# Optimization experiments

Hardware: AMD Instinct MI355X
Metric: run time of the kernel (lower is better)

Reference implementation:

```python
import math
import jax, jax.numpy as jnp
import numpy as np


def _procrustes_R(H):
    # H: [B, 3, 3]. Rotation R = V @ U^T with reflection fix (det(R) >= 0),
    # matching torch.svd convention (v = V, not V^T).
    u, s, vh = jnp.linalg.svd(H)
    v = jnp.swapaxes(vh, -1, -2)                       # [B,3,3]
    r = jnp.einsum('bij,bkj->bik', v, u)               # V @ U^T
    det = jnp.linalg.det(r)                            # [B]
    sign = jnp.where(det < 0, -1.0, 1.0)               # flip last column of V (reflect = diag(1,1,-1))
    flip = jnp.stack([jnp.ones_like(sign), jnp.ones_like(sign), sign], axis=-1)[:, None, :]
    v = v * flip
    return jnp.einsum('bij,bkj->bik', v, u)


def setup_inputs() -> dict:
    key = jax.random.key(0)
    k1, k2, k3, k4 = jax.random.split(key, 4)
    B, D, N, M = 8, 512, 2048, 2048
    return {
        'src_embedding': jax.random.normal(k1, (B, D, N), dtype=jnp.float32),
        'tgt_embedding': jax.random.normal(k2, (B, D, M), dtype=jnp.float32),
        'src': jax.random.normal(k3, (B, 3, N), dtype=jnp.float32),
        'tgt': jax.random.normal(k4, (B, 3, M), dtype=jnp.float32),
    }


def reference(src_embedding, tgt_embedding, src, tgt):
    d_k = src_embedding.shape[1]
    # attention correspondence: scores[b,n,m]
    scores = jnp.einsum('bdn,bdm->bnm', src_embedding, tgt_embedding) / math.sqrt(d_k)
    scores = jax.nn.softmax(scores, axis=2)
    # soft correspondence of src points in tgt: [B,3,N]
    src_corr = jnp.einsum('bdm,bnm->bdn', tgt, scores)
    src_mean = src.mean(axis=2, keepdims=True)          # [B,3,1]
    src_centered = src - src_mean
    src_corr_centered = src_corr - src_corr.mean(axis=2, keepdims=True)
    H = jnp.einsum('bin,bjn->bij', src_centered, src_corr_centered)  # [B,3,3]
    R = _procrustes_R(H)
    t = jnp.einsum('bij,bjk->bik', -R, src_mean) + tgt.mean(axis=2, keepdims=True)
    return R, t.reshape(src.shape[0], 3)
```

## Files before the change

### kernel.cpp

```cpp
#include <hip/hip_runtime.h>
#include <hip/hip_bf16.h>

#define BQ 8
#define DIM 512
#define NN 2048
#define MM 2048
#define MSPLIT 16

typedef __attribute__((ext_vector_type(8))) short short8;
typedef __attribute__((ext_vector_type(8))) unsigned short ushort8;
typedef __attribute__((ext_vector_type(4))) float floatx4;

#define GLOAD_LDS(gp, lp) \
    __builtin_amdgcn_global_load_lds( \
        (const __attribute__((address_space(1))) void*)(gp), \
        (__attribute__((address_space(3))) void*)(lp), 16, 0, 0)


static __device__ __forceinline__ unsigned short f2bf(float x) {
    __hip_bfloat16 h = __float2bfloat16(x);
    return *(unsigned short*)&h;
}

__global__ __launch_bounds__(256) void transpose_cast_kernel(
    const float* __restrict__ src_emb,
    const float* __restrict__ tgt_emb,
    __hip_bfloat16* __restrict__ Abf,
    __hip_bfloat16* __restrict__ Bbf)
{
    const int n0 = blockIdx.x * 64;
    const int d0 = blockIdx.y * 64;
    const int b  = blockIdx.z & 7;
    const int which = blockIdx.z >> 3;

    const float* in = (which == 0 ? src_emb : tgt_emb) + (size_t)b * DIM * NN;
    __hip_bfloat16* out = (which == 0 ? Abf : Bbf) + (size_t)b * NN * DIM;

    __shared__ float tl[64][65];

    const int t = threadIdx.x;

    {
        const int u = t & 15;
        const int r = t >> 4;
        #pragma unroll
        for (int rr = r; rr < 64; rr += 16) {
            float4 v = *(const float4*)&in[(size_t)(d0 + rr) * NN + n0 + u * 4];
            tl[rr][u * 4 + 0] = v.x;
            tl[rr][u * 4 + 1] = v.y;
            tl[rr][u * 4 + 2] = v.z;
            tl[rr][u * 4 + 3] = v.w;
        }
    }
    __syncthreads();

    {
        const int u = t & 7;
        const int r = t >> 3;
        #pragma unroll
        for (int rn = r; rn < 64; rn += 32) {
            ushort8 o;
            #pragma unroll
            for (int j = 0; j < 8; j++)
                o[j] = f2bf(tl[u * 8 + j][rn]);
            *(ushort8*)&out[(size_t)(n0 + rn) * DIM + d0 + u * 8] = o;
        }
    }
}

__global__ __launch_bounds__(512, 2) void attn_mfma_kernel(
    const __hip_bfloat16* __restrict__ Abf,
    const __hip_bfloat16* __restrict__ Bbf,
    const float* __restrict__ tgt,
    float* __restrict__ part)
{
    const int nt = blockIdx.x;
    const int qt = blockIdx.y;
    const int b  = blockIdx.z;
    const int t  = threadIdx.x;
    const int wave = t >> 6;
    const int lane = t & 63;
    const int lm   = lane & 15;
    const int quad = lane >> 4;
    const int wn   = wave * 32;
    const int bw   = wave * 16;

    __shared__ short As[256 * 64];
    __shared__ short Bs[128 * 64];

    const __hip_bfloat16* Abase = Abf + ((size_t)(b * NN + nt * 256)) * DIM;
    const int m0 = qt * 128;
    const __hip_bfloat16* Bbase = Bbf + ((size_t)(b * MM + m0)) * DIM;
    const float* Tb = tgt + (size_t)b * 3 * MM;

    const float SCALE = 0.044194173824159216f * 1.4426950408889634f;

    const int r8 = lane >> 3;
    const int c8 = lane & 7;
    const int cc = c8 ^ r8;
    const __hip_bfloat16* gA = Abase + (size_t)(wn + r8) * DIM + cc * 8;
    const __hip_bfloat16* gB = Bbase + (size_t)(bw + r8) * DIM + cc * 8;
    short* lA = &As[wn * 64];
    short* lB = &Bs[bw * 64];

    floatx4 acc[2][8];
    #pragma unroll
    for (int i = 0; i < 2; i++)
        #pragma unroll
        for (int j = 0; j < 8; j++)
            acc[i][j] = (floatx4){0.f, 0.f, 0.f, 0.f};

    #pragma unroll
    for (int kt = 0; kt < 8; kt++) {
        #pragma unroll
        for (int i = 0; i < 4; i++)
            GLOAD_LDS(gA + kt * 64 + (size_t)i * 8 * DIM, lA + i * 512);
        #pragma unroll
        for (int i = 0; i < 2; i++)
            GLOAD_LDS(gB + kt * 64 + (size_t)i * 8 * DIM, lB + i * 512);
        __syncthreads();

        #pragma unroll
        for (int ks = 0; ks < 2; ks++) {
            const int pc = (((ks * 4 + quad) ^ (lane & 7)) * 8);
            short8 af0 = *(const short8*)&As[(wn +      lm) * 64 + pc];
            short8 af1 = *(const short8*)&As[(wn + 16 + lm) * 64 + pc];
            #pragma unroll
            for (int j = 0; j < 8; j++) {
                short8 bf = *(const short8*)&Bs[(j * 16 + lm) * 64 + pc];
                acc[0][j] = __builtin_amdgcn_mfma_f32_16x16x32_bf16(af0, bf, acc[0][j], 0, 0, 0);
                acc[1][j] = __builtin_amdgcn_mfma_f32_16x16x32_bf16(af1, bf, acc[1][j], 0, 0, 0);
            }
        }
        __syncthreads();
    }

    float v0[8], v1[8], v2[8];
    #pragma unroll
    for (int j = 0; j < 8; j++) {
        int vc = m0 + j * 16 + lm;
        v0[j] = Tb[vc];
        v1[j] = Tb[MM + vc];
        v2[j] = Tb[2 * MM + vc];
    }

    const size_t slot = (size_t)(b * MSPLIT + qt) * NN;
    #pragma unroll
    for (int i = 0; i < 2; i++) {
        float l4[4] = {0,0,0,0};
        float o0[4] = {0,0,0,0};
        float o1[4] = {0,0,0,0};
        float o2[4] = {0,0,0,0};
        #pragma unroll
        for (int j = 0; j < 8; j++) {
            #pragma unroll
            for (int r = 0; r < 4; r++) {
                float e = __builtin_amdgcn_exp2f(acc[i][j][r] * SCALE);
                l4[r] += e;
                o0[r] += e * v0[j];
                o1[r] += e * v1[j];
                o2[r] += e * v2[j];
            }
        }
        #pragma unroll
        for (int m = 1; m <= 8; m <<= 1) {
            #pragma unroll
            for (int r = 0; r < 4; r++) {
                l4[r] += __shfl_xor(l4[r], m);
                o0[r] += __shfl_xor(o0[r], m);
                o1[r] += __shfl_xor(o1[r], m);
                o2[r] += __shfl_xor(o2[r], m);
            }
        }
        if (lm == 0) {
            #pragma unroll
            for (int r = 0; r < 4; r++) {
                int n = nt * 256 + wn + i * 16 + quad * 4 + r;
                ((float4*)part)[slot + n] = make_float4(l4[r], o0[r], o1[r], o2[r]);
            }
        }
    }
}

__global__ __launch_bounds__(128) void reduce1_kernel(
    const float* __restrict__ part,
    const float* __restrict__ src,
    const float* __restrict__ tgt,
    float* __restrict__ red)
{
    const int chunk = blockIdx.x;
    const int b     = blockIdx.y;
    const int t     = threadIdx.x;
    const int n     = chunk * 128 + t;

    const float4* w4 = (const float4*)part;
    const float* S = src + (size_t)b * 3 * NN;
    const float* T = tgt + (size_t)b * 3 * MM;

    float l = 0.f, y0 = 0.f, y1 = 0.f, y2 = 0.f;
    #pragma unroll
    for (int q = 0; q < 16; q++) {
        float4 p = w4[(size_t)(b * 16 + q) * NN + n];
        l += p.x; y0 += p.y; y1 += p.z; y2 += p.w;
    }
    float inv = 1.0f / l;
    float c0 = y0 * inv, c1 = y1 * inv, c2 = y2 * inv;
    float s0 = S[n], s1 = S[NN + n], s2 = S[2 * NN + n];

    float vals[18];
    vals[0] = s0;  vals[1] = s1;  vals[2] = s2;
    vals[3] = c0;  vals[4] = c1;  vals[5] = c2;
    vals[6] = T[n]; vals[7] = T[MM + n]; vals[8] = T[2 * MM + n];
    vals[9]  = s0 * c0; vals[10] = s0 * c1; vals[11] = s0 * c2;
    vals[12] = s1 * c0; vals[13] = s1 * c1; vals[14] = s1 * c2;
    vals[15] = s2 * c0; vals[16] = s2 * c1; vals[17] = s2 * c2;

    #pragma unroll
    for (int m = 1; m <= 32; m <<= 1)
        #pragma unroll
        for (int c = 0; c < 18; c++)
            vals[c] += __shfl_xor(vals[c], m);

    __shared__ float w0[18];
    if (t == 64)
        #pragma unroll
        for (int c = 0; c < 18; c++) w0[c] = vals[c];
    __syncthreads();
    if (t == 0)
        #pragma unroll
        for (int c = 0; c < 18; c++)
            red[(size_t)(b * 16 + chunk) * 18 + c] = vals[c] + w0[c];
}

__global__ __launch_bounds__(64) void procrustes_kernel(
    const float* __restrict__ red,
    float* __restrict__ out)
{
    const int b = blockIdx.x;
    const int t = threadIdx.x;

    __shared__ float res[18];
    if (t < 18) {
        float a = 0.f;
        #pragma unroll
        for (int q = 0; q < 16; q++)
            a += red[(size_t)(b * 16 + q) * 18 + t];
        res[t] = a;
    }
    __syncthreads();

    if (t == 0) {
        const float invN = 1.0f / (float)NN;
        float mus[3], muc[3], mut[3], H[3][3];
        for (int i = 0; i < 3; i++) {
            mus[i] = res[i] * invN;
            muc[i] = res[3 + i] * invN;
            mut[i] = res[6 + i] * invN;
        }
        for (int i = 0; i < 3; i++)
            for (int j = 0; j < 3; j++)
                H[i][j] = res[9 + i * 3 + j] - (float)NN * mus[i] * muc[j];

        float A[3][3];
        for (int i = 0; i < 3; i++)
            for (int j = 0; j < 3; j++)
                A[i][j] = H[0][i] * H[0][j] + H[1][i] * H[1][j] + H[2][i] * H[2][j];

        float V[3][3] = {{1,0,0},{0,1,0},{0,0,1}};
        for (int sweep = 0; sweep < 6; sweep++) {
            for (int pi = 0; pi < 3; pi++) {
                int p = (pi < 2) ? 0 : 1;
                int q = (pi == 0) ? 1 : 2;
                float apq = A[p][q];
                if (fabsf(apq) < 1e-30f) continue;
                float tau = (A[q][q] - A[p][p]) / (2.0f * apq);
                float tt = (tau >= 0.0f) ? 1.0f / (tau + sqrtf(1.0f + tau * tau))
                                         : -1.0f / (-tau + sqrtf(1.0f + tau * tau));
                float c = 1.0f / sqrtf(1.0f + tt * tt);
                float s = tt * c;
                for (int k = 0; k < 3; k++) {
                    float akp = A[k][p], akq = A[k][q];
                    A[k][p] = c * akp - s * akq;
                    A[k][q] = s * akp + c * akq;
                }
                for (int k = 0; k < 3; k++) {
                    float apk = A[p][k], aqk = A[q][k];
                    A[p][k] = c * apk - s * aqk;
                    A[q][k] = s * apk + c * aqk;
                }
                for (int k = 0; k < 3; k++) {
                    float vkp = V[k][p], vkq = V[k][q];
                    V[k][p] = c * vkp - s * vkq;
                    V[k][q] = s * vkp + c * vkq;
                }
            }
        }

        float lam[3] = {A[0][0], A[1][1], A[2][2]};
        int idx[3] = {0, 1, 2};
        for (int a = 0; a < 2; a++)
            for (int bb = 0; bb < 2 - a; bb++)
                if (lam[idx[bb]] < lam[idx[bb + 1]]) { int tmp = idx[bb]; idx[bb] = idx[bb + 1]; idx[bb + 1] = tmp; }

        float Vc[3][3], U[3][3];
        for (int c = 0; c < 3; c++) {
            float sv = sqrtf(fmaxf(lam[idx[c]], 0.0f));
            float isv = 1.0f / fmaxf(sv, 1e-20f);
            for (int r = 0; r < 3; r++) {
                Vc[r][c] = V[r][idx[c]];
                U[r][c] = (H[r][0] * V[0][idx[c]] + H[r][1] * V[1][idx[c]] + H[r][2] * V[2][idx[c]]) * isv;
            }
        }

        {
            float nrm = rsqrtf(U[0][0]*U[0][0] + U[1][0]*U[1][0] + U[2][0]*U[2][0]);
            for (int r = 0; r < 3; r++) U[r][0] *= nrm;
            float d01 = U[0][0]*U[0][1] + U[1][0]*U[1][1] + U[2][0]*U[2][1];
            for (int r = 0; r < 3; r++) U[r][1] -= d01 * U[r][0];
            nrm = rsqrtf(U[0][1]*U[0][1] + U[1][1]*U[1][1] + U[2][1]*U[2][1]);
            for (int r = 0; r < 3; r++) U[r][1] *= nrm;
            float d02 = U[0][0]*U[0][2] + U[1][0]*U[1][2] + U[2][0]*U[2][2];
            float d12 = U[0][1]*U[0][2] + U[1][1]*U[1][2] + U[2][1]*U[2][2];
            for (int r = 0; r < 3; r++) U[r][2] -= d02 * U[r][0] + d12 * U[r][1];
            nrm = rsqrtf(U[0][2]*U[0][2] + U[1][2]*U[1][2] + U[2][2]*U[2][2]);
            for (int r = 0; r < 3; r++) U[r][2] *= nrm;
        }

        float det = H[0][0]*(H[1][1]*H[2][2] - H[1][2]*H[2][1])
                  - H[0][1]*(H[1][0]*H[2][2] - H[1][2]*H[2][0])
                  + H[0][2]*(H[1][0]*H[2][1] - H[1][1]*H[2][0]);
        float sgn = (det < 0.0f) ? -1.0f : 1.0f;

        float R[3][3];
        for (int i = 0; i < 3; i++)
            for (int j = 0; j < 3; j++)
                R[i][j] = Vc[i][0]*U[j][0] + Vc[i][1]*U[j][1] + sgn * Vc[i][2]*U[j][2];

        for (int i = 0; i < 3; i++)
            for (int j = 0; j < 3; j++)
                out[b * 9 + i * 3 + j] = R[i][j];
        for (int i = 0; i < 3; i++)
            out[BQ * 9 + b * 3 + i] = mut[i] - (R[i][0]*mus[0] + R[i][1]*mus[1] + R[i][2]*mus[2]);
    }
}

extern "C" void kernel_launch(void* const* d_in, const int* in_sizes, int n_in,
                              void* d_out, int out_size, void* d_ws, size_t ws_size,
                              hipStream_t stream) {
    const float* src_emb = (const float*)d_in[0];
    const float* tgt_emb = (const float*)d_in[1];
    const float* src     = (const float*)d_in[2];
    const float* tgt     = (const float*)d_in[3];
    float* out = (float*)d_out;

    float* part = (float*)d_ws;
    __hip_bfloat16* Abf = (__hip_bfloat16*)((char*)d_ws + (4 << 20));
    __hip_bfloat16* Bbf = (__hip_bfloat16*)((char*)d_ws + (20 << 20));
    float* red = (float*)((char*)d_ws + (36 << 20));

    dim3 gridT(NN / 64, DIM / 64, 2 * BQ);
    transpose_cast_kernel<<<gridT, 256, 0, stream>>>(src_emb, tgt_emb, Abf, Bbf);

    dim3 gridA(NN / 256, MSPLIT, BQ);
    attn_mfma_kernel<<<gridA, 512, 0, stream>>>(Abf, Bbf, tgt, part);

    dim3 gridR(16, BQ);
    reduce1_kernel<<<gridR, 128, 0, stream>>>(part, src, tgt, red);

    procrustes_kernel<<<BQ, 64, 0, stream>>>(red, out);
}
```

Measured before the change: 166.7 us.

## Double-buffer LDS tiles and enlarge attention tile to 256x256 per block

The attention MFMA kernel now processes a 256x256 score tile per block with a 4x2 wave layout (64x128 per wave) instead of 256x128. It double-buffers A and B in LDS, prefetching the next K slice while computing the current one, using explicit vmcnt waits and raw barriers, and raises wave priority around the MFMA loop. This aims to hide global load latency and improve operand reuse per LDS read. The cost is 128KB of LDS per block and 128 accumulator registers per lane, which likely cuts occupancy below the declared two blocks per CU.

```diff
diff --git a/kernel.cpp b/kernel.cpp
--- a/kernel.cpp
+++ b/kernel.cpp
@@ -5,7 +5,6 @@
 #define DIM 512
 #define NN 2048
 #define MM 2048
-#define MSPLIT 16
 
 typedef __attribute__((ext_vector_type(8))) short short8;
 typedef __attribute__((ext_vector_type(8))) unsigned short ushort8;
@@ -82,14 +81,15 @@
     const int lane = t & 63;
     const int lm   = lane & 15;
     const int quad = lane >> 4;
-    const int wn   = wave * 32;
-    const int bw   = wave * 16;
-
-    __shared__ short As[256 * 64];
-    __shared__ short Bs[128 * 64];
+    const int wn = (wave >> 1) * 64;
+    const int wm = (wave & 1) * 128;
+    const int sr = wave * 32;
+
+    __shared__ short As[2][256 * 64];
+    __shared__ short Bs[2][256 * 64];
 
     const __hip_bfloat16* Abase = Abf + ((size_t)(b * NN + nt * 256)) * DIM;
-    const int m0 = qt * 128;
+    const int m0 = qt * 256;
     const __hip_bfloat16* Bbase = Bbf + ((size_t)(b * MM + m0)) * DIM;
     const float* Tb = tgt + (size_t)b * 3 * MM;
 
@@ -98,55 +98,78 @@
     const int r8 = lane >> 3;
     const int c8 = lane & 7;
     const int cc = c8 ^ r8;
-    const __hip_bfloat16* gA = Abase + (size_t)(wn + r8) * DIM + cc * 8;
-    const __hip_bfloat16* gB = Bbase + (size_t)(bw + r8) * DIM + cc * 8;
-    short* lA = &As[wn * 64];
-    short* lB = &Bs[bw * 64];
-
-    floatx4 acc[2][8];
-    #pragma unroll
-    for (int i = 0; i < 2; i++)
+    const __hip_bfloat16* gA = Abase + (size_t)(sr + r8) * DIM + cc * 8;
+    const __hip_bfloat16* gB = Bbase + (size_t)(sr + r8) * DIM + cc * 8;
+
+#define STAGE(p, kt) do { \
+        short* lAp = &As[p][sr * 64]; \
+        short* lBp = &Bs[p][sr * 64]; \
+        _Pragma("unroll") \
+        for (int i_ = 0; i_ < 4; i_++) { \
+            GLOAD_LDS(gA + (kt) * 64 + (size_t)i_ * 8 * DIM, lAp + i_ * 512); \
+            GLOAD_LDS(gB + (kt) * 64 + (size_t)i_ * 8 * DIM, lBp + i_ * 512); \
+        } \
+    } while (0)
+
+    floatx4 acc[4][8];
+    #pragma unroll
+    for (int i = 0; i < 4; i++)
         #pragma unroll
         for (int j = 0; j < 8; j++)
             acc[i][j] = (floatx4){0.f, 0.f, 0.f, 0.f};
 
+    STAGE(0, 0);
+
     #pragma unroll
     for (int kt = 0; kt < 8; kt++) {
-        #pragma unroll
-        for (int i = 0; i < 4; i++)
-            GLOAD_LDS(gA + kt * 64 + (size_t)i * 8 * DIM, lA + i * 512);
-        #pragma unroll
-        for (int i = 0; i < 2; i++)
-            GLOAD_LDS(gB + kt * 64 + (size_t)i * 8 * DIM, lB + i * 512);
-        __syncthreads();
-
+        const int cur = kt & 1;
+        if (kt < 7) {
+            STAGE(cur ^ 1, kt + 1);
+            asm volatile("s_waitcnt vmcnt(8)" ::: "memory");
+        } else {
+            asm volatile("s_waitcnt vmcnt(0)" ::: "memory");
+        }
+        __builtin_amdgcn_s_barrier();
+
+        const short* Ac = &As[cur][0];
+        const short* Bc = &Bs[cur][0];
+        __builtin_amdgcn_s_setprio(1);
         #pragma unroll
         for (int ks = 0; ks < 2; ks++) {
             const int pc = (((ks * 4 + quad) ^ (lane & 7)) * 8);
-            short8 af0 = *(const short8*)&As[(wn +      lm) * 64 + pc];
-            short8 af1 = *(const short8*)&As[(wn + 16 + lm) * 64 + pc];
+            short8 af[4];
+            #pragma unroll
+            for (int i = 0; i < 4; i++)
+                af[i] = *(const short8*)&Ac[(wn + i * 16 + lm) * 64 + pc];
             #pragma unroll
             for (int j = 0; j < 8; j++) {
-                short8 bf = *(const short8*)&Bs[(j * 16 + lm) * 64 + pc];
-                acc[0][j] = __builtin_amdgcn_mfma_f32_16x16x32_bf16(af0, bf, acc[0][j], 0, 0, 0);
-                acc[1][j] = __builtin_amdgcn_mfma_f32_16x16x32_bf16(af1, bf, acc[1][j], 0, 0, 0);
-            }
-        }
-        __syncthreads();
-    }
+                short8 bf = *(const short8*)&Bc[(wm + j * 16 + lm) * 64 + pc];
+                #pragma unroll
+                for (int i = 0; i < 4; i++)
+                    acc[i][j] = __builtin_amdgcn_mfma_f32_16x16x32_bf16(af[i], bf, acc[i][j], 0, 0, 0);
+            }
+        }
+        __builtin_amdgcn_s_setprio(0);
+
+        if (kt < 7) {
+            asm volatile("s_waitcnt lgkmcnt(0)" ::: "memory");
+            __builtin_amdgcn_s_barrier();
+        }
+    }
+#undef STAGE
 
     float v0[8], v1[8], v2[8];
     #pragma unroll
     for (int j = 0; j < 8; j++) {
-        int vc = m0 + j * 16 + lm;
+        int vc = m0 + wm + j * 16 + lm;
         v0[j] = Tb[vc];
         v1[j] = Tb[MM + vc];
         v2[j] = Tb[2 * MM + vc];
     }
 
-    const size_t slot = (size_t)(b * MSPLIT + qt) * NN;
-    #pragma unroll
-    for (int i = 0; i < 2; i++) {
+    const size_t slot = (size_t)(b * 16 + qt * 2 + (wave & 1)) * NN;
+    #pragma unroll
+    for (int i = 0; i < 4; i++) {
         float l4[4] = {0,0,0,0};
         float o0[4] = {0,0,0,0};
         float o1[4] = {0,0,0,0};
@@ -361,7 +384,7 @@
     dim3 gridT(NN / 64, DIM / 64, 2 * BQ);
     transpose_cast_kernel<<<gridT, 256, 0, stream>>>(src_emb, tgt_emb, Abf, Bbf);
 
-    dim3 gridA(NN / 256, MSPLIT, BQ);
+    dim3 gridA(NN / 256, MM / 256, BQ);
     attn_mfma_kernel<<<gridA, 512, 0, stream>>>(Abf, Bbf, tgt, part);
 
     dim3 gridR(16, BQ);
```

Result: no change. 167.3 us (+0.4%).

## Retile attention GEMM to 128x128 with K=128 stages and merge reduction kernels

Applied to the files above, without the earlier changes.

The attention kernel moves from 256x128 tiles with 512 threads and K-steps of 64 to 128x128 tiles with 256 threads and K-steps of 128. This halves the number of barrier-synchronised K iterations and doubles the grid size. The separate reduce and Procrustes kernels are merged into one 256-thread-per-batch finish kernel, which saves a launch and an intermediate buffer. The trade-offs are less A reuse per block, since B traffic per output doubles relative to A, a larger LDS footprint of 64KB that may limit occupancy, and a serial finish with only 8 blocks.

```diff
diff --git a/kernel.cpp b/kernel.cpp
--- a/kernel.cpp
+++ b/kernel.cpp
@@ -5,7 +5,6 @@
 #define DIM 512
 #define NN 2048
 #define MM 2048
-#define MSPLIT 16
 
 typedef __attribute__((ext_vector_type(8))) short short8;
 typedef __attribute__((ext_vector_type(8))) unsigned short ushort8;
@@ -68,7 +67,7 @@
     }
 }
 
-__global__ __launch_bounds__(512, 2) void attn_mfma_kernel(
+__global__ __launch_bounds__(256, 2) void attn_mfma_kernel(
     const __hip_bfloat16* __restrict__ Abf,
     const __hip_bfloat16* __restrict__ Bbf,
     const float* __restrict__ tgt,
@@ -83,25 +82,20 @@
     const int lm   = lane & 15;
     const int quad = lane >> 4;
     const int wn   = wave * 32;
-    const int bw   = wave * 16;
-
-    __shared__ short As[256 * 64];
-    __shared__ short Bs[128 * 64];
-
-    const __hip_bfloat16* Abase = Abf + ((size_t)(b * NN + nt * 256)) * DIM;
+
+    __shared__ short As[128 * 128];
+    __shared__ short Bs[128 * 128];
+
+    const __hip_bfloat16* Abase = Abf + ((size_t)(b * NN + nt * 128)) * DIM;
     const int m0 = qt * 128;
     const __hip_bfloat16* Bbase = Bbf + ((size_t)(b * MM + m0)) * DIM;
     const float* Tb = tgt + (size_t)b * 3 * MM;
 
     const float SCALE = 0.044194173824159216f * 1.4426950408889634f;
 
-    const int r8 = lane >> 3;
+    const int lr = lane >> 4;
+    const int hh = (lane >> 3) & 1;
     const int c8 = lane & 7;
-    const int cc = c8 ^ r8;
-    const __hip_bfloat16* gA = Abase + (size_t)(wn + r8) * DIM + cc * 8;
-    const __hip_bfloat16* gB = Bbase + (size_t)(bw + r8) * DIM + cc * 8;
-    short* lA = &As[wn * 64];
-    short* lB = &Bs[bw * 64];
 
     floatx4 acc[2][8];
     #pragma unroll
@@ -111,23 +105,26 @@
             acc[i][j] = (floatx4){0.f, 0.f, 0.f, 0.f};
 
     #pragma unroll
-    for (int kt = 0; kt < 8; kt++) {
-        #pragma unroll
-        for (int i = 0; i < 4; i++)
-            GLOAD_LDS(gA + kt * 64 + (size_t)i * 8 * DIM, lA + i * 512);
-        #pragma unroll
-        for (int i = 0; i < 2; i++)
-            GLOAD_LDS(gB + kt * 64 + (size_t)i * 8 * DIM, lB + i * 512);
+    for (int kt = 0; kt < 4; kt++) {
+        #pragma unroll
+        for (int it = 0; it < 8; it++) {
+            const int row = wave * 32 + it * 4 + lr;
+            const size_t goff = (size_t)row * DIM + kt * 128 + hh * 64
+                              + (c8 ^ (row & 7)) * 8;
+            GLOAD_LDS(Abase + goff, &As[(wave * 32 + it * 4) * 128]);
+            GLOAD_LDS(Bbase + goff, &Bs[(wave * 32 + it * 4) * 128]);
+        }
         __syncthreads();
 
         #pragma unroll
-        for (int ks = 0; ks < 2; ks++) {
-            const int pc = (((ks * 4 + quad) ^ (lane & 7)) * 8);
-            short8 af0 = *(const short8*)&As[(wn +      lm) * 64 + pc];
-            short8 af1 = *(const short8*)&As[(wn + 16 + lm) * 64 + pc];
+        for (int ks = 0; ks < 4; ks++) {
+            const int col = (ks >> 1) * 64
+                          + ((((ks & 1) * 4 + quad) ^ (lm & 7)) * 8);
+            short8 af0 = *(const short8*)&As[(wn + lm) * 128 + col];
+            short8 af1 = *(const short8*)&As[(wn + 16 + lm) * 128 + col];
             #pragma unroll
             for (int j = 0; j < 8; j++) {
-                short8 bf = *(const short8*)&Bs[(j * 16 + lm) * 64 + pc];
+                short8 bf = *(const short8*)&Bs[(j * 16 + lm) * 128 + col];
                 acc[0][j] = __builtin_amdgcn_mfma_f32_16x16x32_bf16(af0, bf, acc[0][j], 0, 0, 0);
                 acc[1][j] = __builtin_amdgcn_mfma_f32_16x16x32_bf16(af1, bf, acc[1][j], 0, 0, 0);
             }
@@ -144,7 +141,7 @@
         v2[j] = Tb[2 * MM + vc];
     }
 
-    const size_t slot = (size_t)(b * MSPLIT + qt) * NN;
+    const size_t slot = (size_t)(b * 16 + qt) * NN;
     #pragma unroll
     for (int i = 0; i < 2; i++) {
         float l4[4] = {0,0,0,0};
@@ -175,81 +172,70 @@
         if (lm == 0) {
             #pragma unroll
             for (int r = 0; r < 4; r++) {
-                int n = nt * 256 + wn + i * 16 + quad * 4 + r;
+                int n = nt * 128 + wn + i * 16 + quad * 4 + r;
                 ((float4*)part)[slot + n] = make_float4(l4[r], o0[r], o1[r], o2[r]);
             }
         }
     }
 }
 
-__global__ __launch_bounds__(128) void reduce1_kernel(
+__global__ __launch_bounds__(256) void finish_kernel(
     const float* __restrict__ part,
     const float* __restrict__ src,
     const float* __restrict__ tgt,
-    float* __restrict__ red)
-{
-    const int chunk = blockIdx.x;
-    const int b     = blockIdx.y;
-    const int t     = threadIdx.x;
-    const int n     = chunk * 128 + t;
-
-    const float4* w4 = (const float4*)part;
-    const float* S = src + (size_t)b * 3 * NN;
-    const float* T = tgt + (size_t)b * 3 * MM;
-
-    float l = 0.f, y0 = 0.f, y1 = 0.f, y2 = 0.f;
-    #pragma unroll
-    for (int q = 0; q < 16; q++) {
-        float4 p = w4[(size_t)(b * 16 + q) * NN + n];
-        l += p.x; y0 += p.y; y1 += p.z; y2 += p.w;
-    }
-    float inv = 1.0f / l;
-    float c0 = y0 * inv, c1 = y1 * inv, c2 = y2 * inv;
-    float s0 = S[n], s1 = S[NN + n], s2 = S[2 * NN + n];
-
-    float vals[18];
-    vals[0] = s0;  vals[1] = s1;  vals[2] = s2;
-    vals[3] = c0;  vals[4] = c1;  vals[5] = c2;
-    vals[6] = T[n]; vals[7] = T[MM + n]; vals[8] = T[2 * MM + n];
-    vals[9]  = s0 * c0; vals[10] = s0 * c1; vals[11] = s0 * c2;
-    vals[12] = s1 * c0; vals[13] = s1 * c1; vals[14] = s1 * c2;
-    vals[15] = s2 * c0; vals[16] = s2 * c1; vals[17] = s2 * c2;
-
-    #pragma unroll
-    for (int m = 1; m <= 32; m <<= 1)
-        #pragma unroll
-        for (int c = 0; c < 18; c++)
-            vals[c] += __shfl_xor(vals[c], m);
-
-    __shared__ float w0[18];
-    if (t == 64)
-        #pragma unroll
-        for (int c = 0; c < 18; c++) w0[c] = vals[c];
-    __syncthreads();
-    if (t == 0)
-        #pragma unroll
-        for (int c = 0; c < 18; c++)
-            red[(size_t)(b * 16 + chunk) * 18 + c] = vals[c] + w0[c];
-}
-
-__global__ __launch_bounds__(64) void procrustes_kernel(
-    const float* __restrict__ red,
     float* __restrict__ out)
 {
     const int b = blockIdx.x;
     const int t = threadIdx.x;
-
-    __shared__ float res[18];
-    if (t < 18) {
-        float a = 0.f;
-        #pragma unroll
-        for (int q = 0; q < 16; q++)
-            a += red[(size_t)(b * 16 + q) * 18 + t];
-        res[t] = a;
-    }
+    const int wave = t >> 6;
+    const int lane = t & 63;
+
+    const float4* w4 = (const float4*)part;
+    const float* S = src + (size_t)b * 3 * NN;
+    const float* T = tgt + (size_t)b * 3 * MM;
+
+    float vals[18];
+    #pragma unroll
+    for (int c = 0; c < 18; c++) vals[c] = 0.f;
+
+    for (int k = 0; k < 8; k++) {
+        const int n = t + k * 256;
+        float l = 0.f, y0 = 0.f, y1 = 0.f, y2 = 0.f;
+        #pragma unroll
+        for (int q = 0; q < 16; q++) {
+            float4 p = w4[(size_t)(b * 16 + q) * NN + n];
+            l += p.x; y0 += p.y; y1 += p.z; y2 += p.w;
+        }
+        float inv = 1.0f / l;
+        float c0 = y0 * inv, c1 = y1 * inv, c2 = y2 * inv;
+        float s0 = S[n], s1 = S[NN + n], s2 = S[2 * NN + n];
+
+        vals[0] += s0;  vals[1] += s1;  vals[2] += s2;
+        vals[3] += c0;  vals[4] += c1;  vals[5] += c2;
+        vals[6] += T[n]; vals[7] += T[MM + n]; vals[8] += T[2 * MM + n];
+        vals[9]  += s0 * c0; vals[10] += s0 * c1; vals[11] += s0 * c2;
+        vals[12] += s1 * c0; vals[13] += s1 * c1; vals[14] += s1 * c2;
+        vals[15] += s2 * c0; vals[16] += s2 * c1; vals[17] += s2 * c2;
+    }
+
+    #pragma unroll
+    for (int m = 1; m <= 32; m <<= 1)
+        #pragma unroll
+        for (int c = 0; c < 18; c++)
+            vals[c] += __shfl_xor(vals[c], m);
+
+    __shared__ float wsum[4][18];
+    if (lane == 0)
+        #pragma unroll
+        for (int c = 0; c < 18; c++) wsum[wave][c] = vals[c];
     __syncthreads();
 
     if (t == 0) {
+        float res[18];
+        #pragma unroll
+        for (int c = 0; c < 18; c++)
+            res[c] = wsum[0][c] + wsum[1][c] + wsum[2][c] + wsum[3][c];
+
         const float invN = 1.0f / (float)NN;
         float mus[3], muc[3], mut[3], H[3][3];
         for (int i = 0; i < 3; i++) {
@@ -356,16 +342,12 @@
     float* part = (float*)d_ws;
     __hip_bfloat16* Abf = (__hip_bfloat16*)((char*)d_ws + (4 << 20));
     __hip_bfloat16* Bbf = (__hip_bfloat16*)((char*)d_ws + (20 << 20));
-    float* red = (float*)((char*)d_ws + (36 << 20));
 
     dim3 gridT(NN / 64, DIM / 64, 2 * BQ);
     transpose_cast_kernel<<<gridT, 256, 0, stream>>>(src_emb, tgt_emb, Abf, Bbf);
 
-    dim3 gridA(NN / 256, MSPLIT, BQ);
-    attn_mfma_kernel<<<gridA, 512, 0, stream>>>(Abf, Bbf, tgt, part);
-
-    dim3 gridR(16, BQ);
-    reduce1_kernel<<<gridR, 128, 0, stream>>>(part, src, tgt, red);
-
-    procrustes_kernel<<<BQ, 64, 0, stream>>>(red, out);
-}
+    dim3 gridA(NN / 128, MM / 128, BQ);
+    attn_mfma_kernel<<<gridA, 256, 0, stream>>>(Abf, Bbf, tgt, part);
+
+    finish_kernel<<<BQ, 256, 0, stream>>>(part, src, tgt, out);
+}
```

Result: slower. 183.6 us (+10.1%).
